# Kernel optimization log

Hardware: AMD Instinct MI355X
Metric: run time of the kernel (lower is better)

The kernel has to match this reference:

```python
import jax, jax.numpy as jnp
import numpy as np

B, IN, HID, OUT = 65536, 256, 256, 256


def _xavier(key, shape):
    # shape = (4, fan_in, fan_out); matches torch xavier_uniform_ on [out,in] weight
    fan_in, fan_out = shape[1], shape[2]
    limit = float(np.sqrt(6.0 / (fan_in + fan_out)))
    return jax.random.uniform(key, shape, jnp.float32, -limit, limit)


def setup_inputs() -> dict:
    key = jax.random.key(0)
    ks = jax.random.split(key, 5)
    X = jax.random.normal(ks[0], (B, IN), jnp.float32)
    phi = jax.random.uniform(ks[1], (B,), jnp.float32, minval=0.0, maxval=2.0 * np.pi)
    W1 = _xavier(ks[2], (4, IN, HID))   # stored as [expert, in, out] = W.T per expert
    W2 = _xavier(ks[3], (4, HID, HID))
    W3 = _xavier(ks[4], (4, HID, OUT))
    b1 = jnp.zeros((4, HID), jnp.float32)
    b2 = jnp.zeros((4, HID), jnp.float32)
    b3 = jnp.zeros((4, OUT), jnp.float32)
    return {"X": X, "phi": phi, "W1": W1, "b1": b1, "W2": W2, "b2": b2, "W3": W3, "b3": b3}


def _phase_mix(w):
    """Per-sample expert indices k[i]:[4,B] int32 and cubic coefficients coeff[i]:[4,B]."""
    wi = w.astype(jnp.int32) % 4                      # trunc toward zero, nonneg mod (matches torch)
    k = jnp.stack([(wi - 1) % 4, wi % 4, (wi + 1) % 4, (wi + 2) % 4])  # [4,B]
    w2, w3 = w * w, w * w * w
    coeff = jnp.stack([
        -0.5 * w + w2 - 0.5 * w3,
        -2.5 * w2 + 1.5 * w3,
        0.5 * w + 2.0 * w2 - 1.5 * w3,
        -0.5 * w2 + 0.5 * w3,
    ])                                                # [4,B]
    return k, coeff


def _cyclic_layer(x, W, b, k, coeff):
    # Run all 4 experts batched, then per-sample gather + weighted combine.
    all_out = jnp.einsum('bi,eio->ebo', x, W) + b[:, None, :]  # [4,B,out]
    rows = jnp.arange(x.shape[0])
    out = jnp.zeros((x.shape[0], W.shape[2]), x.dtype)
    for i in range(4):
        out = out + coeff[i][:, None] * all_out[k[i], rows]    # gather expert k[i][b] for sample b
    return out


def reference(X, phi, W1, b1, W2, b2, W3, b3):
    w = (2.0 / jnp.pi) * phi
    k, coeff = _phase_mix(w)
    H1 = jax.nn.relu(_cyclic_layer(X, W1, b1, k, coeff))
    H2 = jax.nn.relu(_cyclic_layer(H1, W2, b2, k, coeff))
    H3 = _cyclic_layer(H2, W3, b3, k, coeff)  # no activation on final layer
    return H3
```

## Files before the change

kernel.cpp:

```cpp
#include <hip/hip_runtime.h>
#include <math.h>

#define NB 65536
#define DIM 256

#define ROWB   528
#define ESEC   18432
#define STAGEB 73728
#define LAYB   589824

typedef _Float16 half8  __attribute__((ext_vector_type(8)));
typedef _Float16 half2v __attribute__((ext_vector_type(2)));
typedef float    f32x4  __attribute__((ext_vector_type(4)));

__global__ __launch_bounds__(256) void convert_w(
    const float* __restrict__ W1, const float* __restrict__ W2,
    const float* __restrict__ W3, char* __restrict__ W16T)
{
  const int g  = blockIdx.x * 256 + threadIdx.x;
  const int n  = g & 255;
  const int k8 = (g >> 8) & 31;
  const int e  = (g >> 13) & 3;
  const int L  = g >> 15;
  const float* WL  = (L == 0) ? W1 : (L == 1) ? W2 : W3;
  const float* src = WL + (size_t)e * DIM * DIM + (size_t)k8 * 8 * DIM + n;
  half8 h;
  #pragma unroll
  for (int j = 0; j < 8; ++j) h[j] = (_Float16)src[(size_t)j * DIM];
  *(half8*)(W16T + (size_t)L * LAYB + (size_t)(n >> 5) * STAGEB
            + e * ESEC + (n & 31) * ROWB + k8 * 16) = h;
}

template<bool WF16, bool IN_F16, bool OUT_F16, bool RELU>
__global__ __launch_bounds__(512, 2) void moe_layer(
    const void* __restrict__ Xin_,
    const float* __restrict__ phi,
    const float* __restrict__ Wf32,
    const char* __restrict__ W16,
    const float* __restrict__ bias,
    void* __restrict__ Out_,
    float acc_scale, float store_scale)
{
  __shared__ __attribute__((aligned(16))) char sStage[2][STAGEB];
  __shared__ float sC[256][4];
  __shared__ float sBias[4][DIM];

  const int tid  = threadIdx.x;
  const int row0 = blockIdx.x * 256;
  const int wave = tid >> 6;
  const int lane = tid & 63;
  const int quad = lane >> 4;
  const int l15  = lane & 15;

  int rowId[4], colId[4];
  {
    half8 vone, vlan;
    #pragma unroll
    for (int j = 0; j < 8; ++j) {
      vone[j] = (_Float16)1.0f;
      vlan[j] = (_Float16)(float)l15;
    }
    const f32x4 z4 = {0.f, 0.f, 0.f, 0.f};
    const f32x4 pm = __builtin_amdgcn_mfma_f32_16x16x32_f16(vlan, vone, z4, 0, 0, 0);
    const f32x4 pn = __builtin_amdgcn_mfma_f32_16x16x32_f16(vone, vlan, z4, 0, 0, 0);
    #pragma unroll
    for (int r = 0; r < 4; ++r) {
      rowId[r] = ((int)(pm[r] * 0.03125f + 0.5f)) & 15;
      colId[r] = ((int)(pn[r] * 0.03125f + 0.5f)) & 15;
    }
  }

  auto stage = [&](int buf, int nt_) {
    if constexpr (WF16) {
      const char* g_ = W16 + (size_t)nt_ * STAGEB + wave * 9216 + lane * 16;
      char*       l_ = &sStage[buf][wave * 9216];
      #pragma unroll
      for (int j = 0; j < 9; ++j)
        __builtin_amdgcn_global_load_lds(
            (const __attribute__((address_space(1))) unsigned int*)(g_ + j * 1024),
            (__attribute__((address_space(3))) unsigned int*)(l_ + j * 1024),
            16, 0, 0);
    } else {
      char* sb = &sStage[buf][0];
      #pragma unroll
      for (int it = 0; it < 8; ++it) {
        const int p  = it * 512 + tid;
        const int e  = p >> 10;
        const int k2 = (p & 1023) >> 3;
        const int ng = p & 7;
        const float* Wp = Wf32 + (size_t)e * DIM * DIM
                        + (size_t)(k2 * 2) * DIM + nt_ * 32 + ng * 4;
        const float4 v0 = *(const float4*)Wp;
        const float4 v1 = *(const float4*)(Wp + DIM);
        const float s0[4] = {v0.x, v0.y, v0.z, v0.w};
        const float s1[4] = {v1.x, v1.y, v1.z, v1.w};
        #pragma unroll
        for (int j = 0; j < 4; ++j) {
          const int n = ng * 4 + j;
          half2v h;
          h[0] = (_Float16)s0[j];
          h[1] = (_Float16)s1[j];
          *(half2v*)(sb + e * ESEC + n * ROWB + k2 * 4) = h;
        }
      }
    }
  };

  stage(0, 0);

  if (tid < 256) {
    const float w  = phi[row0 + tid] * (float)(2.0 / M_PI);
    const int   wi = (int)w;
    const float w2 = w * w, w3 = w2 * w;
    const float cf[4] = {
      -0.5f * w + w2 - 0.5f * w3,
      -2.5f * w2 + 1.5f * w3,
       0.5f * w + 2.0f * w2 - 1.5f * w3,
      -0.5f * w2 + 0.5f * w3 };
    #pragma unroll
    for (int e = 0; e < 4; ++e) sC[tid][e] = cf[(e + 1 - wi) & 3];
  }
  #pragma unroll
  for (int i = tid; i < 4 * DIM; i += 512) sBias[i >> 8][i & 255] = bias[i];

  half8 afr[2][8];
  #pragma unroll
  for (int m = 0; m < 2; ++m) {
    const size_t row = (size_t)(row0 + wave * 32 + m * 16 + l15);
    if constexpr (IN_F16) {
      const _Float16* xr = (const _Float16*)Xin_ + row * DIM;
      #pragma unroll
      for (int kb = 0; kb < 8; ++kb)
        afr[m][kb] = *(const half8*)(xr + kb * 32 + quad * 8);
    } else {
      const float* xr = (const float*)Xin_ + row * DIM;
      #pragma unroll
      for (int kb = 0; kb < 8; ++kb) {
        const float4 a = *(const float4*)(xr + kb * 32 + quad * 8);
        const float4 b = *(const float4*)(xr + kb * 32 + quad * 8 + 4);
        half8 h;
        h[0] = (_Float16)a.x; h[1] = (_Float16)a.y;
        h[2] = (_Float16)a.z; h[3] = (_Float16)a.w;
        h[4] = (_Float16)b.x; h[5] = (_Float16)b.y;
        h[6] = (_Float16)b.z; h[7] = (_Float16)b.w;
        afr[m][kb] = h;
      }
    }
  }

  __syncthreads();

  float creg[2][4][4];
  #pragma unroll
  for (int m = 0; m < 2; ++m)
    #pragma unroll
    for (int r = 0; r < 4; ++r) {
      const int rl = wave * 32 + m * 16 + rowId[r];
      #pragma unroll
      for (int e = 0; e < 4; ++e) creg[m][r][e] = sC[rl][e];
    }

  int cur = 0;
  for (int nt = 0; nt < 8; ++nt) {
    if (nt < 7) stage(cur ^ 1, nt + 1);

    const char* sb = &sStage[cur][0];
    float fin[2][2][4];
    #pragma unroll
    for (int m = 0; m < 2; ++m)
      #pragma unroll
      for (int t = 0; t < 2; ++t)
        #pragma unroll
        for (int r = 0; r < 4; ++r) fin[m][t][r] = 0.f;

    #pragma unroll
    for (int e = 0; e < 4; ++e) {
      f32x4 acc[2][2];
      #pragma unroll
      for (int m = 0; m < 2; ++m)
        #pragma unroll
        for (int t = 0; t < 2; ++t) acc[m][t] = (f32x4){0.f, 0.f, 0.f, 0.f};

      #pragma unroll
      for (int kb = 0; kb < 8; ++kb) {
        #pragma unroll
        for (int t = 0; t < 2; ++t) {
          const half8 b = *(const half8*)(sb + e * ESEC + (t * 16 + l15) * ROWB
                                          + kb * 64 + quad * 16);
          acc[0][t] = __builtin_amdgcn_mfma_f32_16x16x32_f16(afr[0][kb], b, acc[0][t], 0, 0, 0);
          acc[1][t] = __builtin_amdgcn_mfma_f32_16x16x32_f16(afr[1][kb], b, acc[1][t], 0, 0, 0);
        }
      }

      #pragma unroll
      for (int m = 0; m < 2; ++m)
        #pragma unroll
        for (int t = 0; t < 2; ++t)
          #pragma unroll
          for (int r = 0; r < 4; ++r)
            fin[m][t][r] += creg[m][r][e] * acc[m][t][r];
    }

    #pragma unroll
    for (int t = 0; t < 2; ++t)
      #pragma unroll
      for (int r = 0; r < 4; ++r) {
        const int n_l = nt * 32 + t * 16 + colId[r];
        float be[4];
        #pragma unroll
        for (int e = 0; e < 4; ++e) be[e] = sBias[e][n_l];
        #pragma unroll
        for (int m = 0; m < 2; ++m) {
          const int row_l = wave * 32 + m * 16 + rowId[r];
          float v = acc_scale * fin[m][t][r];
          #pragma unroll
          for (int e = 0; e < 4; ++e) v += creg[m][r][e] * be[e];
          if (RELU) v = fmaxf(v, 0.f);
          v *= store_scale;
          const size_t idx = (size_t)(row0 + row_l) * DIM + n_l;
          if (OUT_F16) ((_Float16*)Out_)[idx] = (_Float16)v;
          else         ((float*)Out_)[idx] = v;
        }
      }

    __syncthreads();
    cur ^= 1;
  }
}

extern "C" void kernel_launch(void* const* d_in, const int* in_sizes, int n_in,
                              void* d_out, int out_size, void* d_ws, size_t ws_size,
                              hipStream_t stream) {
  const float* X   = (const float*)d_in[0];
  const float* phi = (const float*)d_in[1];
  const float* W1  = (const float*)d_in[2];
  const float* b1  = (const float*)d_in[3];
  const float* W2  = (const float*)d_in[4];
  const float* b2  = (const float*)d_in[5];
  const float* W3  = (const float*)d_in[6];
  const float* b3  = (const float*)d_in[7];

  const size_t h2_bytes  = (size_t)NB * DIM * sizeof(_Float16);
  const size_t w16_bytes = (size_t)3 * LAYB;

  _Float16* H1  = (_Float16*)d_out;
  _Float16* H2;
  char*     W16 = nullptr;
  if (ws_size >= h2_bytes + w16_bytes) {
    H2  = (_Float16*)d_ws;
    W16 = (char*)d_ws + h2_bytes;
  } else if (ws_size >= h2_bytes) {
    H2 = (_Float16*)d_ws;
  } else if (ws_size >= w16_bytes) {
    W16 = (char*)d_ws;
    H2  = (_Float16*)d_in[0];
  } else {
    H2 = (_Float16*)d_in[0];
  }
  float* out = (float*)d_out;

  dim3 grid(NB / 256);
  dim3 block(512);

  if (W16) {
    convert_w<<<dim3(384), dim3(256), 0, stream>>>(W1, W2, W3, W16);
    moe_layer<true, false, true,  true ><<<grid, block, 0, stream>>>(X,  phi, nullptr, W16,            b1, H1,  1.0f, 1.0f);
    moe_layer<true, true,  true,  true ><<<grid, block, 0, stream>>>(H1, phi, nullptr, W16 + LAYB,     b2, H2,  1.0f, 0.125f);
    moe_layer<true, true,  false, false><<<grid, block, 0, stream>>>(H2, phi, nullptr, W16 + 2 * LAYB, b3, out, 8.0f, 1.0f);
  } else {
    moe_layer<false, false, true,  true ><<<grid, block, 0, stream>>>(X,  phi, W1, nullptr, b1, H1,  1.0f, 1.0f);
    moe_layer<false, true,  true,  true ><<<grid, block, 0, stream>>>(H1, phi, W2, nullptr, b2, H2,  1.0f, 0.125f);
    moe_layer<false, true,  false, false><<<grid, block, 0, stream>>>(H2, phi, W3, nullptr, b3, out, 8.0f, 1.0f);
  }
}
```

Baseline: 249.1 us.

## Retile waves to 64 rows by 16 columns and hardcode MFMA output layout

Changes the per-wave tile from 32 rows by 32 columns to 64 rows by 16 columns, so each B fragment read from LDS feeds four MFMAs instead of two. This halves LDS weight reads per MFMA. The cost is doubling the register-resident activation fragments (afr) and coefficient registers. The runtime MFMA probe for row and column indices is replaced by the known layout (quad*4+r rows, lane columns). The barrier is moved before the epilogue stores so the stores can overlap the next stage's loads.

Measured after the change: 245.1 us. No clear change (-1.6%).

```diff
diff --git a/kernel.cpp b/kernel.cpp
--- a/kernel.cpp
+++ b/kernel.cpp
@@ -7,6 +7,7 @@
 #define ROWB   528
 #define ESEC   18432
 #define STAGEB 73728
+#define NTILE  8
 #define LAYB   589824
 
 typedef _Float16 half8  __attribute__((ext_vector_type(8)));
@@ -51,24 +52,8 @@
   const int lane = tid & 63;
   const int quad = lane >> 4;
   const int l15  = lane & 15;
-
-  int rowId[4], colId[4];
-  {
-    half8 vone, vlan;
-    #pragma unroll
-    for (int j = 0; j < 8; ++j) {
-      vone[j] = (_Float16)1.0f;
-      vlan[j] = (_Float16)(float)l15;
-    }
-    const f32x4 z4 = {0.f, 0.f, 0.f, 0.f};
-    const f32x4 pm = __builtin_amdgcn_mfma_f32_16x16x32_f16(vlan, vone, z4, 0, 0, 0);
-    const f32x4 pn = __builtin_amdgcn_mfma_f32_16x16x32_f16(vone, vlan, z4, 0, 0, 0);
-    #pragma unroll
-    for (int r = 0; r < 4; ++r) {
-      rowId[r] = ((int)(pm[r] * 0.03125f + 0.5f)) & 15;
-      colId[r] = ((int)(pn[r] * 0.03125f + 0.5f)) & 15;
-    }
-  }
+  const int ms   = wave & 3;
+  const int cs   = wave >> 2;
 
   auto stage = [&](int buf, int nt_) {
     if constexpr (WF16) {
@@ -96,11 +81,10 @@
         const float s1[4] = {v1.x, v1.y, v1.z, v1.w};
         #pragma unroll
         for (int j = 0; j < 4; ++j) {
-          const int n = ng * 4 + j;
           half2v h;
           h[0] = (_Float16)s0[j];
           h[1] = (_Float16)s1[j];
-          *(half2v*)(sb + e * ESEC + n * ROWB + k2 * 4) = h;
+          *(half2v*)(sb + e * ESEC + (ng * 4 + j) * ROWB + k2 * 4) = h;
         }
       }
     }
@@ -123,10 +107,10 @@
   #pragma unroll
   for (int i = tid; i < 4 * DIM; i += 512) sBias[i >> 8][i & 255] = bias[i];
 
-  half8 afr[2][8];
-  #pragma unroll
-  for (int m = 0; m < 2; ++m) {
-    const size_t row = (size_t)(row0 + wave * 32 + m * 16 + l15);
+  half8 afr[4][8];
+  #pragma unroll
+  for (int m = 0; m < 4; ++m) {
+    const size_t row = (size_t)(row0 + ms * 64 + m * 16 + l15);
     if constexpr (IN_F16) {
       const _Float16* xr = (const _Float16*)Xin_ + row * DIM;
       #pragma unroll
@@ -150,80 +134,71 @@
 
   __syncthreads();
 
-  float creg[2][4][4];
-  #pragma unroll
-  for (int m = 0; m < 2; ++m)
+  float creg[4][4][4];
+  #pragma unroll
+  for (int m = 0; m < 4; ++m)
     #pragma unroll
     for (int r = 0; r < 4; ++r) {
-      const int rl = wave * 32 + m * 16 + rowId[r];
+      const int rl = ms * 64 + m * 16 + quad * 4 + r;
       #pragma unroll
       for (int e = 0; e < 4; ++e) creg[m][r][e] = sC[rl][e];
     }
 
   int cur = 0;
-  for (int nt = 0; nt < 8; ++nt) {
-    if (nt < 7) stage(cur ^ 1, nt + 1);
+  for (int nt = 0; nt < NTILE; ++nt) {
+    if (nt < NTILE - 1) stage(cur ^ 1, nt + 1);
 
     const char* sb = &sStage[cur][0];
-    float fin[2][2][4];
-    #pragma unroll
-    for (int m = 0; m < 2; ++m)
-      #pragma unroll
-      for (int t = 0; t < 2; ++t)
+    float fin[4][4];
+    #pragma unroll
+    for (int m = 0; m < 4; ++m)
+      #pragma unroll
+      for (int r = 0; r < 4; ++r) fin[m][r] = 0.f;
+
+    #pragma unroll
+    for (int e = 0; e < 4; ++e) {
+      f32x4 acc[4];
+      #pragma unroll
+      for (int m = 0; m < 4; ++m) acc[m] = (f32x4){0.f, 0.f, 0.f, 0.f};
+
+      #pragma unroll
+      for (int kb = 0; kb < 8; ++kb) {
+        const half8 b = *(const half8*)(sb + e * ESEC + (cs * 16 + l15) * ROWB
+                                        + kb * 64 + quad * 16);
+        acc[0] = __builtin_amdgcn_mfma_f32_16x16x32_f16(afr[0][kb], b, acc[0], 0, 0, 0);
+        acc[1] = __builtin_amdgcn_mfma_f32_16x16x32_f16(afr[1][kb], b, acc[1], 0, 0, 0);
+        acc[2] = __builtin_amdgcn_mfma_f32_16x16x32_f16(afr[2][kb], b, acc[2], 0, 0, 0);
+        acc[3] = __builtin_amdgcn_mfma_f32_16x16x32_f16(afr[3][kb], b, acc[3], 0, 0, 0);
+      }
+
+      #pragma unroll
+      for (int m = 0; m < 4; ++m)
         #pragma unroll
-        for (int r = 0; r < 4; ++r) fin[m][t][r] = 0.f;
-
-    #pragma unroll
-    for (int e = 0; e < 4; ++e) {
-      f32x4 acc[2][2];
-      #pragma unroll
-      for (int m = 0; m < 2; ++m)
+        for (int r = 0; r < 4; ++r)
+          fin[m][r] += creg[m][r][e] * acc[m][r];
+    }
+
+    __syncthreads();
+
+    const int n_l = nt * 32 + cs * 16 + l15;
+    float be[4];
+    #pragma unroll
+    for (int e = 0; e < 4; ++e) be[e] = sBias[e][n_l];
+    #pragma unroll
+    for (int m = 0; m < 4; ++m)
+      #pragma unroll
+      for (int r = 0; r < 4; ++r) {
+        const int row_l = ms * 64 + m * 16 + quad * 4 + r;
+        float v = acc_scale * fin[m][r];
         #pragma unroll
-        for (int t = 0; t < 2; ++t) acc[m][t] = (f32x4){0.f, 0.f, 0.f, 0.f};
-
-      #pragma unroll
-      for (int kb = 0; kb < 8; ++kb) {
-        #pragma unroll
-        for (int t = 0; t < 2; ++t) {
-          const half8 b = *(const half8*)(sb + e * ESEC + (t * 16 + l15) * ROWB
-                                          + kb * 64 + quad * 16);
-          acc[0][t] = __builtin_amdgcn_mfma_f32_16x16x32_f16(afr[0][kb], b, acc[0][t], 0, 0, 0);
-          acc[1][t] = __builtin_amdgcn_mfma_f32_16x16x32_f16(afr[1][kb], b, acc[1][t], 0, 0, 0);
-        }
-      }
-
-      #pragma unroll
-      for (int m = 0; m < 2; ++m)
-        #pragma unroll
-        for (int t = 0; t < 2; ++t)
-          #pragma unroll
-          for (int r = 0; r < 4; ++r)
-            fin[m][t][r] += creg[m][r][e] * acc[m][t][r];
-    }
-
-    #pragma unroll
-    for (int t = 0; t < 2; ++t)
-      #pragma unroll
-      for (int r = 0; r < 4; ++r) {
-        const int n_l = nt * 32 + t * 16 + colId[r];
-        float be[4];
-        #pragma unroll
-        for (int e = 0; e < 4; ++e) be[e] = sBias[e][n_l];
-        #pragma unroll
-        for (int m = 0; m < 2; ++m) {
-          const int row_l = wave * 32 + m * 16 + rowId[r];
-          float v = acc_scale * fin[m][t][r];
-          #pragma unroll
-          for (int e = 0; e < 4; ++e) v += creg[m][r][e] * be[e];
-          if (RELU) v = fmaxf(v, 0.f);
-          v *= store_scale;
-          const size_t idx = (size_t)(row0 + row_l) * DIM + n_l;
-          if (OUT_F16) ((_Float16*)Out_)[idx] = (_Float16)v;
-          else         ((float*)Out_)[idx] = v;
-        }
-      }
-
-    __syncthreads();
+        for (int e = 0; e < 4; ++e) v += creg[m][r][e] * be[e];
+        if (RELU) v = fmaxf(v, 0.f);
+        v *= store_scale;
+        const size_t idx = (size_t)(row0 + row_l) * DIM + n_l;
+        if (OUT_F16) ((_Float16*)Out_)[idx] = (_Float16)v;
+        else         ((float*)Out_)[idx] = v;
+      }
+
     cur ^= 1;
   }
 }
```
